# Kernel optimization log

Hardware: AMD Instinct MI355X
Metric: run time of the kernel (lower is better)

## Reference

```python
import jax, jax.numpy as jnp
import numpy as np

BATCH, SEQ_LEN, INPUT_SIZE, HIDDEN_SIZE = 64, 512, 1024, 1024


def setup_inputs() -> dict:
    key = jax.random.key(0)
    ks = jax.random.split(key, 9)
    def xavier(k, shape):
        # matches nn.init.xavier_uniform_
        limit = jnp.sqrt(6.0 / (shape[0] + shape[1])).astype(jnp.float32)
        return jax.random.uniform(k, shape, jnp.float32, -limit, limit)
    x = jax.random.normal(ks[0], (BATCH, SEQ_LEN, INPUT_SIZE), jnp.float32)
    return {
        "x": x,
        "w_f": xavier(ks[1], (INPUT_SIZE, HIDDEN_SIZE)),
        "u_f": xavier(ks[2], (HIDDEN_SIZE, HIDDEN_SIZE)),
        "b_f": jnp.zeros((HIDDEN_SIZE,), jnp.float32),
        "w_i": xavier(ks[3], (INPUT_SIZE, HIDDEN_SIZE)),
        "u_i": xavier(ks[4], (HIDDEN_SIZE, HIDDEN_SIZE)),
        "b_i": jnp.zeros((HIDDEN_SIZE,), jnp.float32),
        "w_o": xavier(ks[5], (INPUT_SIZE, HIDDEN_SIZE)),
        "u_o": xavier(ks[6], (HIDDEN_SIZE, HIDDEN_SIZE)),
        "b_o": jnp.zeros((HIDDEN_SIZE,), jnp.float32),
        "w_c": xavier(ks[7], (INPUT_SIZE, HIDDEN_SIZE)),
        "u_c": xavier(ks[8], (HIDDEN_SIZE, HIDDEN_SIZE)),
        "b_c": jnp.zeros((HIDDEN_SIZE,), jnp.float32),
    }


def reference(x, w_f, u_f, b_f, w_i, u_i, b_i, w_o, u_o, b_o, w_c, u_c, b_c):
    B, S, _ = x.shape
    H = w_f.shape[1]
    # Precompute input projections for all timesteps (same math, one big GEMM each)
    xf = jnp.einsum('bsd,dh->bsh', x, w_f) + b_f
    xi = jnp.einsum('bsd,dh->bsh', x, w_i) + b_i
    xo = jnp.einsum('bsd,dh->bsh', x, w_o) + b_o
    xc = jnp.einsum('bsd,dh->bsh', x, w_c) + b_c
    # time-major for scan: [S, B, H]
    xs = (jnp.swapaxes(xf, 0, 1), jnp.swapaxes(xi, 0, 1),
          jnp.swapaxes(xo, 0, 1), jnp.swapaxes(xc, 0, 1))

    def step(carry, xt):
        h, c = carry
        xft, xit, xot, xct = xt
        f = jax.nn.sigmoid(xft + h @ u_f)
        i = jax.nn.sigmoid(xit + h @ u_i)
        o = jax.nn.sigmoid(xot + h @ u_o)
        c = f * c + i * jnp.tanh(xct + h @ u_c)
        h = o * jnp.tanh(c)
        return (h, c), h

    h0 = jnp.zeros((B, H), x.dtype)
    c0 = jnp.zeros((B, H), x.dtype)
    (h, c), ys = jax.lax.scan(step, (h0, c0), xs)
    ys = jnp.swapaxes(ys, 0, 1)  # [B, S, H]
    return ys, (h, c)
```

## Files before the change

kernel.cpp:

```cpp
#include <hip/hip_runtime.h>
#include <hip/hip_cooperative_groups.h>
#include <stdint.h>

namespace cg = cooperative_groups;

typedef __attribute__((ext_vector_type(8))) short short8;
typedef __attribute__((ext_vector_type(4))) float floatx4;

#define DI __device__ __forceinline__

constexpr int BB = 64;
constexpr int SS = 512;
constexpr int II = 1024;
constexpr int HH = 1024;
constexpr int MM = BB * SS;
constexpr int NN = 4 * HH;

DI unsigned short f2bf(float f) {
  union { float f; unsigned int u; } v; v.f = f;
  unsigned int u = v.u;
  return (unsigned short)((u + 0x7FFFu + ((u >> 16) & 1u)) >> 16);
}
DI float bf2f(unsigned short u) {
  union { unsigned int u; float f; } v; v.u = ((unsigned int)u) << 16;
  return v.f;
}
DI float sigmoidf_(float x) { return 1.0f / (1.0f + __expf(-x)); }
DI float tanhf_(float x)    { return 2.0f / (1.0f + __expf(-2.0f * x)) - 1.0f; }

DI void gload_lds16(const unsigned short* g, unsigned short* l) {
  typedef __attribute__((address_space(1))) const void gv_t;
  typedef __attribute__((address_space(3))) void lv_t;
  __builtin_amdgcn_global_load_lds((gv_t*)(uintptr_t)g, (lv_t*)(uintptr_t)l, 16, 0, 0);
}

__global__ __launch_bounds__(256) void k_transpose_cast(
    const float* __restrict__ src, unsigned short* __restrict__ dst) {
  __shared__ float tile[32][33];
  const int bx = blockIdx.x;
  const int n0 = (bx & 31) * 32, k0 = (bx >> 5) * 32;
  const int tx = threadIdx.x & 31, ty = threadIdx.x >> 5;
#pragma unroll
  for (int i = 0; i < 4; ++i)
    tile[ty + i * 8][tx] = src[(size_t)(k0 + ty + i * 8) * 1024 + n0 + tx];
  __syncthreads();
#pragma unroll
  for (int i = 0; i < 4; ++i)
    dst[(size_t)(n0 + ty + i * 8) * 1024 + k0 + tx] = f2bf(tile[tx][ty + i * 8]);
}

__global__ __launch_bounds__(256) void k_cast_x(
    const float* __restrict__ src, unsigned short* __restrict__ dst, int n8) {
  int idx = blockIdx.x * 256 + threadIdx.x;
  if (idx >= n8) return;
  const floatx4* s = (const floatx4*)(src + (size_t)idx * 8);
  floatx4 a = s[0], b = s[1];
  short8 o;
  o[0] = (short)f2bf(a[0]); o[1] = (short)f2bf(a[1]);
  o[2] = (short)f2bf(a[2]); o[3] = (short)f2bf(a[3]);
  o[4] = (short)f2bf(b[0]); o[5] = (short)f2bf(b[1]);
  o[6] = (short)f2bf(b[2]); o[7] = (short)f2bf(b[3]);
  *(short8*)(dst + (size_t)idx * 8) = o;
}

__global__ __launch_bounds__(256) void k_gemm_xw(
    const unsigned short* __restrict__ A,
    const unsigned short* __restrict__ Bt,
    unsigned short* __restrict__ C)
{
  __shared__ unsigned short As[128 * 32];
  __shared__ unsigned short Bs[128 * 32];
  const int bid = blockIdx.x;
  const int bm = bid & 255;
  const int bn = bid >> 8;
  const int m0 = bm * 128, n0 = bn * 128;
  const int tid = threadIdx.x;
  const int lane = tid & 63, wid = tid >> 6;

  const unsigned short* ga = A  + (size_t)(m0 + (tid >> 2)) * 1024 + (tid & 3) * 8;
  const unsigned short* gb = Bt + (size_t)(n0 + (tid >> 2)) * 1024 + (tid & 3) * 8;
  unsigned short* lA = As + wid * 512;
  unsigned short* lB = Bs + wid * 512;

  floatx4 acc[4][4] = {};
  const int wm = (wid >> 1) * 64, wn = (wid & 1) * 64;
  const int lr = lane & 15, lk = (lane >> 4) * 8;

  for (int k0 = 0; k0 < 1024; k0 += 32) {
    gload_lds16(ga + k0, lA);
    gload_lds16(ga + 64 * 1024 + k0, lA + 2048);
    gload_lds16(gb + k0, lB);
    gload_lds16(gb + 64 * 1024 + k0, lB + 2048);
    __syncthreads();
    short8 af[4], bfv[4];
#pragma unroll
    for (int mt = 0; mt < 4; ++mt)
      af[mt] = *(const short8*)(As + (wm + mt * 16 + lr) * 32 + lk);
#pragma unroll
    for (int nt = 0; nt < 4; ++nt)
      bfv[nt] = *(const short8*)(Bs + (wn + nt * 16 + lr) * 32 + lk);
#pragma unroll
    for (int mt = 0; mt < 4; ++mt)
#pragma unroll
      for (int nt = 0; nt < 4; ++nt)
        acc[mt][nt] = __builtin_amdgcn_mfma_f32_16x16x32_bf16(
            af[mt], bfv[nt], acc[mt][nt], 0, 0, 0);
    __syncthreads();
  }

#pragma unroll
  for (int mt = 0; mt < 4; ++mt) {
    const int row = m0 + wm + mt * 16 + (lane >> 4) * 4;
#pragma unroll
    for (int nt = 0; nt < 4; ++nt) {
      const int col = n0 + wn + nt * 16 + lr;
      unsigned short* cp = C + (size_t)row * 4096 + col;
#pragma unroll
      for (int r = 0; r < 4; ++r)
        cp[(size_t)r * 4096] = f2bf(acc[mt][nt][r]);
    }
  }
}

__global__ __launch_bounds__(256) void k_recurrence(
    const unsigned short* __restrict__ gates,
    const unsigned short* __restrict__ Ut,
    const float* __restrict__ bF, const float* __restrict__ bI,
    const float* __restrict__ bO, const float* __restrict__ bC,
    unsigned short* __restrict__ hbuf,
    float* __restrict__ out)
{
  __shared__ float part[4][16][68];
  cg::grid_group grid = cg::this_grid();

  const int bid = blockIdx.x;
  const int jswz = (bid & 7) * 32 + (bid >> 3);
  const int col0 = jswz * 4;
  const int tid = threadIdx.x, lane = tid & 63, w = tid >> 6;
  const int lr = lane & 15, lk = (lane >> 4) * 8;

  const int nloc = lr, g = nloc >> 2, c = nloc & 3;
  short8 bfrag[8];
  {
    const unsigned short* up = Ut + ((size_t)(g * 1024 + col0 + c)) * 1024 + w * 256 + lk;
#pragma unroll
    for (int ks = 0; ks < 8; ++ks) bfrag[ks] = *(const short8*)(up + ks * 32);
  }

  const int eb = tid >> 2, ecl = tid & 3;
  const int hcol = col0 + ecl;
  const float bias0 = bF[hcol], bias1 = bI[hcol], bias2 = bO[hcol], bias3 = bC[hcol];

  float cstate = 0.0f, hval = 0.0f;

  hbuf[bid * 256 + tid] = 0;
  grid.sync();

  for (int s = 0; s < SS; ++s) {
    const unsigned short* hp = hbuf + (s & 1) * 65536;
    unsigned short* hw = hbuf + ((s & 1) ^ 1) * 65536;

    floatx4 acc[4] = {};
#pragma unroll
    for (int ks = 0; ks < 8; ++ks) {
#pragma unroll
      for (int mt = 0; mt < 4; ++mt) {
        short8 a = *(const short8*)(hp + (size_t)(mt * 16 + lr) * 1024 +
                                    w * 256 + ks * 32 + lk);
        acc[mt] = __builtin_amdgcn_mfma_f32_16x16x32_bf16(a, bfrag[ks], acc[mt], 0, 0, 0);
      }
    }
#pragma unroll
    for (int mt = 0; mt < 4; ++mt)
      *(floatx4*)&part[w][nloc][mt * 16 + (lane >> 4) * 4] = acc[mt];
    __syncthreads();

    float pre[4];
#pragma unroll
    for (int gg = 0; gg < 4; ++gg) {
      int n = gg * 4 + ecl;
      float v = part[0][n][eb] + part[1][n][eb] + part[2][n][eb] + part[3][n][eb];
      float gx = bf2f(gates[(size_t)(eb * 512 + s) * 4096 + gg * 1024 + hcol]);
      pre[gg] = v + gx + ((gg == 0) ? bias0 : (gg == 1) ? bias1 : (gg == 2) ? bias2 : bias3);
    }
    float fg = sigmoidf_(pre[0]);
    float ig = sigmoidf_(pre[1]);
    float og = sigmoidf_(pre[2]);
    float gc = tanhf_(pre[3]);
    cstate = fg * cstate + ig * gc;
    hval = og * tanhf_(cstate);

    hw[eb * 1024 + hcol] = f2bf(hval);
    out[(size_t)(eb * 512 + s) * 1024 + hcol] = hval;

    grid.sync();
  }

  const size_t ys_sz = (size_t)BB * SS * HH;
  out[ys_sz + (size_t)eb * 1024 + hcol] = hval;
  out[ys_sz + 65536 + (size_t)eb * 1024 + hcol] = cstate;
}

extern "C" void kernel_launch(void* const* d_in, const int* in_sizes, int n_in,
                              void* d_out, int out_size, void* d_ws, size_t ws_size,
                              hipStream_t stream) {
  const float* x = (const float*)d_in[0];
  const float* w[4] = { (const float*)d_in[1], (const float*)d_in[4],
                        (const float*)d_in[7], (const float*)d_in[10] };
  const float* u[4] = { (const float*)d_in[2], (const float*)d_in[5],
                        (const float*)d_in[8], (const float*)d_in[11] };
  const float* b[4] = { (const float*)d_in[3], (const float*)d_in[6],
                        (const float*)d_in[9], (const float*)d_in[12] };

  const size_t OFF_WT = 0;
  const size_t OFF_UT = 8u << 20;
  const size_t OFF_XB = 16u << 20;
  const size_t OFF_GX = 80u << 20;
  const size_t OFF_HB = (80u << 20) + (256u << 20);
  const size_t NEED = OFF_HB + 2 * 65536 * 2;
  if (ws_size < NEED) return;

  char* ws = (char*)d_ws;
  unsigned short* Wt = (unsigned short*)(ws + OFF_WT);
  unsigned short* Ut = (unsigned short*)(ws + OFF_UT);
  unsigned short* Xb = (unsigned short*)(ws + OFF_XB);
  unsigned short* Gx = (unsigned short*)(ws + OFF_GX);
  unsigned short* Hb = (unsigned short*)(ws + OFF_HB);

  for (int gi = 0; gi < 4; ++gi) {
    k_transpose_cast<<<1024, 256, 0, stream>>>(w[gi], Wt + (size_t)gi * 1024 * 1024);
    k_transpose_cast<<<1024, 256, 0, stream>>>(u[gi], Ut + (size_t)gi * 1024 * 1024);
  }
  k_cast_x<<<(MM * II / 8) / 256, 256, 0, stream>>>(x, Xb, MM * II / 8);
  k_gemm_xw<<<256 * 32, 256, 0, stream>>>(Xb, Wt, Gx);

  const unsigned short* gx_p = Gx;
  const unsigned short* ut_p = Ut;
  const float* b0 = b[0]; const float* b1 = b[1];
  const float* b2 = b[2]; const float* b3 = b[3];
  unsigned short* hb_p = Hb;
  float* out_p = (float*)d_out;
  void* args[] = { (void*)&gx_p, (void*)&ut_p, (void*)&b0, (void*)&b1,
                   (void*)&b2, (void*)&b3, (void*)&hb_p, (void*)&out_p };
  hipLaunchCooperativeKernel(k_recurrence, dim3(256), dim3(256), args, 0, stream);
}
```

Baseline: 19.36 ms.

## Restructure LSTM recurrence onto 64 blocks with custom atomic grid barrier

Replaces the 256-block cooperative-groups recurrence with a 64-block, 512-thread kernel. Each block owns 16 hidden columns across all four gates, and partial sums are reduced through LDS atomics. The cg grid.sync is swapped for a hand-rolled atomic counter/flag barrier that is reset in the cast kernel. The gate GEMM output is stored time-major, so the per-step gate reads are contiguous and prefetched one step ahead. The aim is to cut per-step grid-sync cost and latency, at the cost of fewer CUs doing the recurrent matmul and LDS atomic contention.

```diff
diff --git a/kernel.cpp b/kernel.cpp
--- a/kernel.cpp
+++ b/kernel.cpp
@@ -1,8 +1,5 @@
 #include <hip/hip_runtime.h>
-#include <hip/hip_cooperative_groups.h>
 #include <stdint.h>
-
-namespace cg = cooperative_groups;
 
 typedef __attribute__((ext_vector_type(8))) short short8;
 typedef __attribute__((ext_vector_type(4))) float floatx4;
@@ -14,7 +11,7 @@
 constexpr int II = 1024;
 constexpr int HH = 1024;
 constexpr int MM = BB * SS;
-constexpr int NN = 4 * HH;
+constexpr int NBLK = 64;
 
 DI unsigned short f2bf(float f) {
   union { float f; unsigned int u; } v; v.f = f;
@@ -32,6 +29,25 @@
   typedef __attribute__((address_space(1))) const void gv_t;
   typedef __attribute__((address_space(3))) void lv_t;
   __builtin_amdgcn_global_load_lds((gv_t*)(uintptr_t)g, (lv_t*)(uintptr_t)l, 16, 0, 0);
+}
+
+DI void grid_barrier(int* bar, int gen) {
+  __syncthreads();
+  if (threadIdx.x == 0) {
+    __threadfence();
+    int old = __hip_atomic_fetch_add(&bar[0], 1, __ATOMIC_RELAXED,
+                                     __HIP_MEMORY_SCOPE_AGENT);
+    if (old == gen * NBLK - 1) {
+      __hip_atomic_store(&bar[1], gen, __ATOMIC_RELEASE,
+                         __HIP_MEMORY_SCOPE_AGENT);
+    } else {
+      while (__hip_atomic_load(&bar[1], __ATOMIC_RELAXED,
+                               __HIP_MEMORY_SCOPE_AGENT) < gen)
+        __builtin_amdgcn_s_sleep(1);
+    }
+    __threadfence();
+  }
+  __syncthreads();
 }
 
 __global__ __launch_bounds__(256) void k_transpose_cast(
@@ -50,7 +66,11 @@
 }
 
 __global__ __launch_bounds__(256) void k_cast_x(
-    const float* __restrict__ src, unsigned short* __restrict__ dst, int n8) {
+    const float* __restrict__ src, unsigned short* __restrict__ dst, int n8,
+    int* __restrict__ bar) {
+  if (blockIdx.x == 0 && threadIdx.x < 2)
+    __hip_atomic_store(&bar[threadIdx.x], 0, __ATOMIC_RELAXED,
+                       __HIP_MEMORY_SCOPE_AGENT);
   int idx = blockIdx.x * 256 + threadIdx.x;
   if (idx >= n8) return;
   const floatx4* s = (const floatx4*)(src + (size_t)idx * 8);
@@ -112,93 +132,145 @@
   for (int mt = 0; mt < 4; ++mt) {
     const int row = m0 + wm + mt * 16 + (lane >> 4) * 4;
 #pragma unroll
-    for (int nt = 0; nt < 4; ++nt) {
-      const int col = n0 + wn + nt * 16 + lr;
-      unsigned short* cp = C + (size_t)row * 4096 + col;
-#pragma unroll
-      for (int r = 0; r < 4; ++r)
-        cp[(size_t)r * 4096] = f2bf(acc[mt][nt][r]);
+    for (int r = 0; r < 4; ++r) {
+      const int rr = row + r;
+      unsigned short* cp = C + (size_t)((rr & 511) * 64 + (rr >> 9)) * 4096;
+#pragma unroll
+      for (int nt = 0; nt < 4; ++nt) {
+        const int col = n0 + wn + nt * 16 + lr;
+        cp[col] = f2bf(acc[mt][nt][r]);
+      }
     }
   }
 }
 
-__global__ __launch_bounds__(256) void k_recurrence(
+__global__ __launch_bounds__(512, 2) void k_recur64(
     const unsigned short* __restrict__ gates,
     const unsigned short* __restrict__ Ut,
     const float* __restrict__ bF, const float* __restrict__ bI,
     const float* __restrict__ bO, const float* __restrict__ bC,
     unsigned short* __restrict__ hbuf,
+    int* __restrict__ bar,
     float* __restrict__ out)
 {
-  __shared__ float part[4][16][68];
-  cg::grid_group grid = cg::this_grid();
-
+  __shared__ float part1[64][69];
   const int bid = blockIdx.x;
-  const int jswz = (bid & 7) * 32 + (bid >> 3);
-  const int col0 = jswz * 4;
-  const int tid = threadIdx.x, lane = tid & 63, w = tid >> 6;
+  const int tid = threadIdx.x;
+  const int lane = tid & 63, w = tid >> 6;
   const int lr = lane & 15, lk = (lane >> 4) * 8;
-
-  const int nloc = lr, g = nloc >> 2, c = nloc & 3;
-  short8 bfrag[8];
-  {
-    const unsigned short* up = Ut + ((size_t)(g * 1024 + col0 + c)) * 1024 + w * 256 + lk;
-#pragma unroll
-    for (int ks = 0; ks < 8; ++ks) bfrag[ks] = *(const short8*)(up + ks * 32);
-  }
-
-  const int eb = tid >> 2, ecl = tid & 3;
-  const int hcol = col0 + ecl;
-  const float bias0 = bF[hcol], bias1 = bI[hcol], bias2 = bO[hcol], bias3 = bC[hcol];
-
-  float cstate = 0.0f, hval = 0.0f;
-
-  hbuf[bid * 256 + tid] = 0;
-  grid.sync();
+  const int hcol0 = bid * 16;
+
+  short8 bfrag[4][4];
+#pragma unroll
+  for (int n = 0; n < 4; ++n) {
+    const unsigned short* up = Ut + ((size_t)n << 20) +
+                               (size_t)(hcol0 + lr) * 1024 + w * 128 + lk;
+#pragma unroll
+    for (int kt = 0; kt < 4; ++kt)
+      bfrag[n][kt] = *(const short8*)(up + kt * 32);
+  }
+
+  const int eb = tid >> 3, ej = tid & 7;
+  const int hc0 = 2 * ej;
+  const int gc = hcol0 + hc0;
+  float2 bias[4];
+  bias[0] = *(const float2*)(bF + gc);
+  bias[1] = *(const float2*)(bI + gc);
+  bias[2] = *(const float2*)(bO + gc);
+  bias[3] = *(const float2*)(bC + gc);
+
+  for (int i = tid; i < 64 * 69; i += 512) ((float*)part1)[i] = 0.0f;
+  *(unsigned int*)(hbuf + eb * 1024 + gc) = 0u;
+
+  float c0 = 0.f, c1 = 0.f, h0v = 0.f, h1v = 0.f;
+  int gen = 1;
+  grid_barrier(bar, gen++);
+
+  unsigned int g_nxt[4];
+#pragma unroll
+  for (int g = 0; g < 4; ++g)
+    g_nxt[g] = *(const unsigned int*)(gates + (size_t)eb * 4096 + g * 1024 + gc);
 
   for (int s = 0; s < SS; ++s) {
     const unsigned short* hp = hbuf + (s & 1) * 65536;
     unsigned short* hw = hbuf + ((s & 1) ^ 1) * 65536;
-
-    floatx4 acc[4] = {};
-#pragma unroll
-    for (int ks = 0; ks < 8; ++ks) {
-#pragma unroll
-      for (int mt = 0; mt < 4; ++mt) {
-        short8 a = *(const short8*)(hp + (size_t)(mt * 16 + lr) * 1024 +
-                                    w * 256 + ks * 32 + lk);
-        acc[mt] = __builtin_amdgcn_mfma_f32_16x16x32_bf16(a, bfrag[ks], acc[mt], 0, 0, 0);
+    unsigned int gcur[4] = { g_nxt[0], g_nxt[1], g_nxt[2], g_nxt[3] };
+
+    floatx4 acc[4][4] = {};
+    const unsigned short* hbase = hp + w * 128 + lk;
+    short8 a0[4], a1[4];
+#pragma unroll
+    for (int mt = 0; mt < 4; ++mt)
+      a0[mt] = *(const short8*)(hbase + (size_t)(mt * 16 + lr) * 1024);
+#pragma unroll
+    for (int kt = 0; kt < 4; ++kt) {
+      const short8* cur = (kt & 1) ? a1 : a0;
+      short8* nxt = (kt & 1) ? a0 : a1;
+      if (kt < 3) {
+#pragma unroll
+        for (int mt = 0; mt < 4; ++mt)
+          nxt[mt] = *(const short8*)(hbase + (kt + 1) * 32 +
+                                     (size_t)(mt * 16 + lr) * 1024);
       }
+#pragma unroll
+      for (int mt = 0; mt < 4; ++mt)
+#pragma unroll
+        for (int n = 0; n < 4; ++n)
+          acc[mt][n] = __builtin_amdgcn_mfma_f32_16x16x32_bf16(
+              cur[mt], bfrag[n][kt], acc[mt][n], 0, 0, 0);
     }
+
+    const int r0 = (lane >> 4) * 4;
 #pragma unroll
     for (int mt = 0; mt < 4; ++mt)
-      *(floatx4*)&part[w][nloc][mt * 16 + (lane >> 4) * 4] = acc[mt];
+#pragma unroll
+      for (int n = 0; n < 4; ++n) {
+        float* p = &part1[n * 16 + lr][mt * 16 + r0];
+#pragma unroll
+        for (int r = 0; r < 4; ++r) atomicAdd(p + r, acc[mt][n][r]);
+      }
+
+    const int sn = (s + 1 < SS) ? s + 1 : s;
+#pragma unroll
+    for (int g = 0; g < 4; ++g)
+      g_nxt[g] = *(const unsigned int*)(gates + ((size_t)sn * 64 + eb) * 4096 +
+                                        g * 1024 + gc);
+
     __syncthreads();
 
-    float pre[4];
-#pragma unroll
-    for (int gg = 0; gg < 4; ++gg) {
-      int n = gg * 4 + ecl;
-      float v = part[0][n][eb] + part[1][n][eb] + part[2][n][eb] + part[3][n][eb];
-      float gx = bf2f(gates[(size_t)(eb * 512 + s) * 4096 + gg * 1024 + hcol]);
-      pre[gg] = v + gx + ((gg == 0) ? bias0 : (gg == 1) ? bias1 : (gg == 2) ? bias2 : bias3);
+    float pre0[4], pre1[4];
+#pragma unroll
+    for (int g = 0; g < 4; ++g) {
+      pre0[g] = part1[g * 16 + hc0][eb] +
+                bf2f((unsigned short)(gcur[g] & 0xffffu)) + bias[g].x;
+      pre1[g] = part1[g * 16 + hc0 + 1][eb] +
+                bf2f((unsigned short)(gcur[g] >> 16)) + bias[g].y;
     }
-    float fg = sigmoidf_(pre[0]);
-    float ig = sigmoidf_(pre[1]);
-    float og = sigmoidf_(pre[2]);
-    float gc = tanhf_(pre[3]);
-    cstate = fg * cstate + ig * gc;
-    hval = og * tanhf_(cstate);
-
-    hw[eb * 1024 + hcol] = f2bf(hval);
-    out[(size_t)(eb * 512 + s) * 1024 + hcol] = hval;
-
-    grid.sync();
+    float f0 = sigmoidf_(pre0[0]), f1 = sigmoidf_(pre1[0]);
+    float i0 = sigmoidf_(pre0[1]), i1 = sigmoidf_(pre1[1]);
+    float o0 = sigmoidf_(pre0[2]), o1 = sigmoidf_(pre1[2]);
+    float q0 = tanhf_(pre0[3]),    q1 = tanhf_(pre1[3]);
+    c0 = f0 * c0 + i0 * q0;  c1 = f1 * c1 + i1 * q1;
+    h0v = o0 * tanhf_(c0);   h1v = o1 * tanhf_(c1);
+
+    __syncthreads();
+    for (int i = tid; i < 64 * 69; i += 512) ((float*)part1)[i] = 0.0f;
+
+    unsigned int hpack = (unsigned int)f2bf(h0v) |
+                         ((unsigned int)f2bf(h1v) << 16);
+    *(unsigned int*)(hw + eb * 1024 + gc) = hpack;
+    float2 yv; yv.x = h0v; yv.y = h1v;
+    __builtin_nontemporal_store(
+        *(double*)&yv, (double*)(out + ((size_t)eb * 512 + s) * 1024 + gc));
+
+    grid_barrier(bar, gen++);
   }
 
   const size_t ys_sz = (size_t)BB * SS * HH;
-  out[ys_sz + (size_t)eb * 1024 + hcol] = hval;
-  out[ys_sz + 65536 + (size_t)eb * 1024 + hcol] = cstate;
+  out[ys_sz + (size_t)eb * 1024 + gc]             = h0v;
+  out[ys_sz + (size_t)eb * 1024 + gc + 1]         = h1v;
+  out[ys_sz + 65536 + (size_t)eb * 1024 + gc]     = c0;
+  out[ys_sz + 65536 + (size_t)eb * 1024 + gc + 1] = c1;
 }
 
 extern "C" void kernel_launch(void* const* d_in, const int* in_sizes, int n_in,
@@ -217,7 +289,8 @@
   const size_t OFF_XB = 16u << 20;
   const size_t OFF_GX = 80u << 20;
   const size_t OFF_HB = (80u << 20) + (256u << 20);
-  const size_t NEED = OFF_HB + 2 * 65536 * 2;
+  const size_t OFF_BAR = OFF_HB + 2 * 65536 * 2;
+  const size_t NEED = OFF_BAR + 256;
   if (ws_size < NEED) return;
 
   char* ws = (char*)d_ws;
@@ -226,12 +299,13 @@
   unsigned short* Xb = (unsigned short*)(ws + OFF_XB);
   unsigned short* Gx = (unsigned short*)(ws + OFF_GX);
   unsigned short* Hb = (unsigned short*)(ws + OFF_HB);
+  int* Bar = (int*)(ws + OFF_BAR);
 
   for (int gi = 0; gi < 4; ++gi) {
     k_transpose_cast<<<1024, 256, 0, stream>>>(w[gi], Wt + (size_t)gi * 1024 * 1024);
     k_transpose_cast<<<1024, 256, 0, stream>>>(u[gi], Ut + (size_t)gi * 1024 * 1024);
   }
-  k_cast_x<<<(MM * II / 8) / 256, 256, 0, stream>>>(x, Xb, MM * II / 8);
+  k_cast_x<<<(MM * II / 8) / 256, 256, 0, stream>>>(x, Xb, MM * II / 8, Bar);
   k_gemm_xw<<<256 * 32, 256, 0, stream>>>(Xb, Wt, Gx);
 
   const unsigned short* gx_p = Gx;
@@ -239,8 +313,10 @@
   const float* b0 = b[0]; const float* b1 = b[1];
   const float* b2 = b[2]; const float* b3 = b[3];
   unsigned short* hb_p = Hb;
+  int* bar_p = Bar;
   float* out_p = (float*)d_out;
   void* args[] = { (void*)&gx_p, (void*)&ut_p, (void*)&b0, (void*)&b1,
-                   (void*)&b2, (void*)&b3, (void*)&hb_p, (void*)&out_p };
-  hipLaunchCooperativeKernel(k_recurrence, dim3(256), dim3(256), args, 0, stream);
-}
+                   (void*)&b2, (void*)&b3, (void*)&hb_p, (void*)&bar_p,
+                   (void*)&out_p };
+  hipLaunchCooperativeKernel(k_recur64, dim3(NBLK), dim3(512), args, 0, stream);
+}
```

Measured after the change: 26.46 ms. +36.6%, slower.
